# Kernel optimization log

Hardware: AMD Instinct MI355X
Metric: run time of the kernel (lower is better)

The kernel has to match this reference:

```python
import jax, jax.numpy as jnp
import numpy as np

NEG_BIG = -9e15

def setup_inputs() -> dict:
    key = jax.random.key(0)
    k1, k2, k3, k4 = jax.random.split(key, 4)
    N, F_in, F_out = 8192, 512, 128
    return {
        "input": jax.random.normal(k1, (N, F_in), dtype=jnp.float32),
        "adj": jax.random.randint(k2, (N, N), 0, 2, dtype=jnp.int32),
        "W": jax.random.normal(k3, (F_in, F_out), dtype=jnp.float32) * 0.05,
        "a": jax.random.normal(k4, (2 * F_out, 1), dtype=jnp.float32) * 0.05,
    }

def reference(input, adj, W, a):
    alpha = 0.2  # LeakyReLU negative slope
    h = input @ W                      # [N, F_out]
    F_out = h.shape[1]
    # concat score decomposition: a^T [h_i || h_j] = h_i @ a1 + h_j @ a2
    a1 = a[:F_out, 0]                  # [F_out]
    a2 = a[F_out:, 0]                  # [F_out]
    e = jax.nn.leaky_relu(h @ a1[:, None] + (h @ a2)[None, :], negative_slope=alpha)  # [N, N]
    e = jnp.where(adj > 0, e, NEG_BIG)
    attention = jax.nn.softmax(e, axis=1)
    h_prime = attention @ h            # [N, F_out]
    return jax.nn.elu(h_prime)         # concat=True
```

## Files before the change

### kernel.cpp

```cpp
#include <hip/hip_runtime.h>
#include <hip/hip_bf16.h>


typedef __attribute__((ext_vector_type(4))) float f32x4;
typedef __attribute__((ext_vector_type(8))) short s16x8;

#define N_NODES 8192
#define F_IN 512
#define F_OUT 128
#define JS 8
#define JCHUNK (N_NODES / JS)

static __device__ __forceinline__ short f2bf(float f) {
  __hip_bfloat16 h = __float2bfloat16(f);
  return __builtin_bit_cast(short, h);
}

__global__ __launch_bounds__(256) void k_mask(const int* __restrict__ adj,
    unsigned long long* __restrict__ mask) {
  const int nwaves = gridDim.x * 4;
  int wid = blockIdx.x * 4 + (threadIdx.x >> 6);
  int lane = threadIdx.x & 63;
  const int ntasks = N_NODES * (N_NODES / 64);
  for (int task = wid; task < ntasks; task += nwaves) {
    int row = task >> 7;
    int cg = task & 127;
    int v = adj[(size_t)row * N_NODES + cg * 64 + lane];
    unsigned long long b = __ballot(v != 0);
    if (lane == 0) mask[(size_t)row * (N_NODES / 64) + cg] = b;
  }
}

__global__ void k0a_wt(const float* __restrict__ W, unsigned short* __restrict__ WT) {
  int idx = blockIdx.x * 256 + threadIdx.x;
  int k = idx >> 7, f = idx & 127;
  WT[(size_t)f * F_IN + k] = (unsigned short)f2bf(W[idx]);
}

__global__ void k0c_wa(const float* __restrict__ W, const float* __restrict__ a,
                       float* __restrict__ wa) {
  int k = blockIdx.x * 256 + threadIdx.x;
  if (k >= F_IN) return;
  const float* Wr = W + (size_t)k * F_OUT;
  float d1 = 0.f, d2 = 0.f;
#pragma unroll 8
  for (int f = 0; f < F_OUT; f += 4) {
    f32x4 w  = *(const f32x4*)(Wr + f);
    f32x4 a1 = *(const f32x4*)(a + f);
    f32x4 a2 = *(const f32x4*)(a + F_OUT + f);
    d1 += w[0] * a1[0] + w[1] * a1[1] + w[2] * a1[2] + w[3] * a1[3];
    d2 += w[0] * a2[0] + w[1] * a2[1] + w[2] * a2[2] + w[3] * a2[3];
  }
  wa[k] = d1;
  wa[F_IN + k] = d2;
}

__global__ __launch_bounds__(256) void k0b_x(const float* __restrict__ X,
    const float* __restrict__ wa, unsigned short* __restrict__ Xb,
    f32x4* __restrict__ rowdat, unsigned* __restrict__ pE) {
  int wave = threadIdx.x >> 6, lane = threadIdx.x & 63;
  int i = blockIdx.x * 4 + wave;
  const float* Xr = X + (size_t)i * F_IN + lane * 8;
  f32x4 x0 = ((const f32x4*)Xr)[0];
  f32x4 x1 = ((const f32x4*)Xr)[1];
  f32x4 w10 = ((const f32x4*)(wa + lane * 8))[0];
  f32x4 w11 = ((const f32x4*)(wa + lane * 8))[1];
  f32x4 w20 = ((const f32x4*)(wa + F_IN + lane * 8))[0];
  f32x4 w21 = ((const f32x4*)(wa + F_IN + lane * 8))[1];

  s16x8 xb;
#pragma unroll
  for (int e = 0; e < 4; e++) { xb[e] = f2bf(x0[e]); xb[e + 4] = f2bf(x1[e]); }
  *(s16x8*)(Xb + (size_t)i * F_IN + lane * 8) = xb;

  float d1 = 0.f, d2 = 0.f;
#pragma unroll
  for (int e = 0; e < 4; e++) {
    d1 += x0[e] * w10[e] + x1[e] * w11[e];
    d2 += x0[e] * w20[e] + x1[e] * w21[e];
  }
#pragma unroll
  for (int m = 1; m < 64; m <<= 1) {
    d1 += __shfl_xor(d1, m, 64);
    d2 += __shfl_xor(d2, m, 64);
  }
  if (lane == 0) {
    float s1 = d1, s2 = d2;
    f32x4 rd;
    rd[0] = expf(s1);
    rd[1] = expf(0.2f * s1);
    rd[2] = expf(-s1);
    rd[3] = 0.f;
    rowdat[i] = rd;
    unsigned e2  = (unsigned)(unsigned short)f2bf(expf(s2));
    unsigned e2s = (unsigned)(unsigned short)f2bf(expf(0.2f * s2));
    pE[i] = (e2s << 16) | e2;
  }
}

__global__ __launch_bounds__(256) void k1_gemm(const unsigned short* __restrict__ WT,
    const unsigned short* __restrict__ Xb, unsigned short* __restrict__ hT) {
  int wave = threadIdx.x >> 6, lane = threadIdx.x & 63;
  int lrow = lane & 15, grp = lane >> 4;
  int tile = blockIdx.x * 4 + wave;
  int fb = tile & 7;
  int nb = tile >> 3;

  const unsigned short* Ar = WT + (size_t)(fb * 16 + lrow) * F_IN + grp * 8;
  const unsigned short* Br = Xb + (size_t)(nb * 16 + lrow) * F_IN + grp * 8;

  f32x4 acc = (f32x4)(0.0f);
#pragma unroll
  for (int k0 = 0; k0 < F_IN; k0 += 32) {
    s16x8 af = *(const s16x8*)(Ar + k0);
    s16x8 bf = *(const s16x8*)(Br + k0);
    acc = __builtin_amdgcn_mfma_f32_16x16x32_bf16(af, bf, acc, 0, 0, 0);
  }
#pragma unroll
  for (int r = 0; r < 4; r++)
    hT[(size_t)(fb * 16 + grp * 4 + r) * N_NODES + nb * 16 + lrow] =
        (unsigned short)f2bf(acc[r]);
}

__global__ __launch_bounds__(256, 4) void k2_main(const unsigned* __restrict__ mask32,
    const unsigned short* __restrict__ hT, const f32x4* __restrict__ rowdat,
    const unsigned* __restrict__ pE, float* __restrict__ accws,
    float* __restrict__ denws) {
  int js = blockIdx.x & (JS - 1);
  int rb = blockIdx.x / JS;
  int wave = threadIdx.x >> 6, lane = threadIdx.x & 63;
  int lrow = lane & 15, grp = lane >> 4;
  int waveRow = rb * 64 + wave * 16;
  int i0 = waveRow + lrow;
  int jlo = js * JCHUNK;

  f32x4 rd = rowdat[i0];
  float E1 = rd[0], E1s = rd[1], T1 = rd[2];

  f32x4 acc[8];
#pragma unroll
  for (int n = 0; n < 8; n++) acc[n] = (f32x4)(0.0f);
  float dsum = 0.f;

#define PROC(pe, e)                                                  \
  {                                                                  \
    unsigned pu = (pe);                                              \
    float E2  = __builtin_bit_cast(float, pu << 16);                 \
    float E2s = __builtin_bit_cast(float, pu & 0xffff0000u);         \
    float sel = (E2 > T1) ? E1 * E2 : E1s * E2s;                     \
    float p = ((b >> e) & 1u) ? sel : 0.f;                           \
    dsum += p;                                                       \
    af[e] = f2bf(p);                                                 \
  }

  for (int sc = 0; sc < JCHUNK / 512; sc++) {
    int jbase = jlo + sc * 512;
    const uint4* mrow =
        (const uint4*)(mask32 + (size_t)i0 * (N_NODES / 32) + jbase / 32);
    uint4 mm[4];
#pragma unroll
    for (int c = 0; c < 4; c++) mm[c] = mrow[c];

#pragma unroll
    for (int t = 0; t < 16; t++) {
      int jj = jbase + t * 32 + grp * 8;
      unsigned b = (mm[t >> 2][t & 3] >> (grp * 8)) & 0xffu;
      const uint4* pp = (const uint4*)(pE + jj);
      uint4 P0 = pp[0], P1 = pp[1];
      s16x8 af;
      PROC(P0.x, 0); PROC(P0.y, 1); PROC(P0.z, 2); PROC(P0.w, 3);
      PROC(P1.x, 4); PROC(P1.y, 5); PROC(P1.z, 6); PROC(P1.w, 7);
      const unsigned short* hTj = hT + jj;
#pragma unroll
      for (int n = 0; n < 8; n++) {
        s16x8 bf = *(const s16x8*)(hTj + (size_t)(n * 16 + lrow) * N_NODES);
        acc[n] = __builtin_amdgcn_mfma_f32_16x16x32_bf16(af, bf, acc[n], 0, 0, 0);
      }
    }
  }
#undef PROC

  dsum += __shfl_xor(dsum, 16, 64);
  dsum += __shfl_xor(dsum, 32, 64);
  if (lane < 16) denws[js * N_NODES + waveRow + lane] = dsum;

#pragma unroll
  for (int n = 0; n < 8; n++)
#pragma unroll
    for (int r = 0; r < 4; r++)
      accws[((size_t)js * N_NODES + waveRow + grp * 4 + r) * F_OUT + n * 16 + lrow] =
          acc[n][r];
}

__global__ void k3_fin(const float* __restrict__ accws,
                       const float* __restrict__ denws, float* __restrict__ out) {
  int idx4 = blockIdx.x * 256 + threadIdx.x;
  int i = idx4 >> 5;
  const int S4 = N_NODES * F_OUT / 4;
  f32x4 s = (f32x4)(0.0f);
  float d = 0.f;
#pragma unroll
  for (int js = 0; js < JS; js++) {
    s += ((const f32x4*)accws)[idx4 + js * S4];
    d += denws[i + js * N_NODES];
  }
  f32x4 v = s / d;
#pragma unroll
  for (int e = 0; e < 4; e++) v[e] = v[e] > 0.f ? v[e] : expm1f(v[e]);
  ((f32x4*)out)[idx4] = v;
}

extern "C" void kernel_launch(void* const* d_in, const int* in_sizes, int n_in,
                              void* d_out, int out_size, void* d_ws, size_t ws_size,
                              hipStream_t stream) {
  const float* X   = (const float*)d_in[0];
  const int*   adj = (const int*)d_in[1];
  const float* W   = (const float*)d_in[2];
  const float* a   = (const float*)d_in[3];
  float* out = (float*)d_out;

  char* ws = (char*)d_ws;
  size_t off = 0;
  unsigned short* WT = (unsigned short*)(ws + off); off += (size_t)F_OUT * F_IN * 2;
  unsigned short* Xb = (unsigned short*)(ws + off); off += (size_t)N_NODES * F_IN * 2;
  unsigned short* hT = (unsigned short*)(ws + off); off += (size_t)F_OUT * N_NODES * 2;
  f32x4* rowdat = (f32x4*)(ws + off); off += (size_t)N_NODES * 16;
  unsigned* pE = (unsigned*)(ws + off); off += (size_t)N_NODES * 4;
  float* wa = (float*)(ws + off); off += (size_t)2 * F_IN * 4;
  unsigned long long* mask = (unsigned long long*)(ws + off);
  off += (size_t)N_NODES * (N_NODES / 64) * 8;
  float* accws = (float*)(ws + off); off += (size_t)JS * N_NODES * F_OUT * 4;
  float* denws = (float*)(ws + off); off += (size_t)JS * N_NODES * 4;
  (void)in_sizes; (void)n_in; (void)out_size; (void)ws_size;

  k_mask<<<2048, 256, 0, stream>>>(adj, mask);
  k0a_wt<<<(F_IN * F_OUT) / 256, 256, 0, stream>>>(W, WT);
  k0c_wa<<<2, 256, 0, stream>>>(W, a, wa);
  k0b_x<<<N_NODES / 4, 256, 0, stream>>>(X, wa, Xb, rowdat, pE);
  k1_gemm<<<1024, 256, 0, stream>>>(WT, Xb, hT);
  k2_main<<<(N_NODES / 64) * JS, 256, 0, stream>>>((const unsigned*)mask, hT,
                                                   rowdat, pE, accws, denws);
  k3_fin<<<(N_NODES * F_OUT) / 4 / 256, 256, 0, stream>>>(accws, denws, out);
}
```

Measured before the change: 552.1 us.

## Give each wave 64 rows to reuse hT fragments across four MFMA row tiles

The main attention kernel now assigns each wave a 64-row by 512-column tile. Each hT B-fragment load feeds four MFMAs instead of one, which cuts global/L2 traffic for hT by about 4x. The j-split grows from 8 to 16, so the partial accumulator workspace and the final reduction double in size. Register use rises from 32 to 128 accumulator floats, and launch bounds drop occupancy to 2 blocks. Separately, the mask-building kernel has each wave handle 256 columns with four ballots and vectorized stores, reducing loop overhead.

```diff
diff --git a/kernel.cpp b/kernel.cpp
--- a/kernel.cpp
+++ b/kernel.cpp
@@ -8,8 +8,8 @@
 #define N_NODES 8192
 #define F_IN 512
 #define F_OUT 128
-#define JS 8
-#define JCHUNK (N_NODES / JS)
+#define JS 16
+#define WCOLS (N_NODES / JS)
 
 static __device__ __forceinline__ short f2bf(float f) {
   __hip_bfloat16 h = __float2bfloat16(f);
@@ -21,13 +21,23 @@
   const int nwaves = gridDim.x * 4;
   int wid = blockIdx.x * 4 + (threadIdx.x >> 6);
   int lane = threadIdx.x & 63;
-  const int ntasks = N_NODES * (N_NODES / 64);
+  const int ntasks = N_NODES * (N_NODES / 256);
   for (int task = wid; task < ntasks; task += nwaves) {
-    int row = task >> 7;
-    int cg = task & 127;
-    int v = adj[(size_t)row * N_NODES + cg * 64 + lane];
-    unsigned long long b = __ballot(v != 0);
-    if (lane == 0) mask[(size_t)row * (N_NODES / 64) + cg] = b;
+    int row = task >> 5;
+    int cg = task & 31;
+    const int* p = adj + (size_t)row * N_NODES + cg * 256 + lane;
+    int v0 = p[0], v1 = p[64], v2 = p[128], v3 = p[192];
+    unsigned long long b0 = __ballot(v0 != 0);
+    unsigned long long b1 = __ballot(v1 != 0);
+    unsigned long long b2 = __ballot(v2 != 0);
+    unsigned long long b3 = __ballot(v3 != 0);
+    if (lane == 0) {
+      unsigned long long* q = mask + (size_t)row * (N_NODES / 64) + cg * 4;
+      ulonglong2 w0; w0.x = b0; w0.y = b1;
+      ulonglong2 w1; w1.x = b2; w1.y = b3;
+      *(ulonglong2*)(q) = w0;
+      *(ulonglong2*)(q + 2) = w1;
+    }
   }
 }
 
@@ -122,74 +132,92 @@
         (unsigned short)f2bf(acc[r]);
 }
 
-__global__ __launch_bounds__(256, 4) void k2_main(const unsigned* __restrict__ mask32,
+__global__ __launch_bounds__(256, 2) void k2_main(const unsigned* __restrict__ mask32,
     const unsigned short* __restrict__ hT, const f32x4* __restrict__ rowdat,
     const unsigned* __restrict__ pE, float* __restrict__ accws,
     float* __restrict__ denws) {
-  int js = blockIdx.x & (JS - 1);
-  int rb = blockIdx.x / JS;
   int wave = threadIdx.x >> 6, lane = threadIdx.x & 63;
   int lrow = lane & 15, grp = lane >> 4;
-  int waveRow = rb * 64 + wave * 16;
-  int i0 = waveRow + lrow;
-  int jlo = js * JCHUNK;
-
-  f32x4 rd = rowdat[i0];
-  float E1 = rd[0], E1s = rd[1], T1 = rd[2];
-
-  f32x4 acc[8];
-#pragma unroll
-  for (int n = 0; n < 8; n++) acc[n] = (f32x4)(0.0f);
-  float dsum = 0.f;
-
-#define PROC(pe, e)                                                  \
-  {                                                                  \
-    unsigned pu = (pe);                                              \
-    float E2  = __builtin_bit_cast(float, pu << 16);                 \
-    float E2s = __builtin_bit_cast(float, pu & 0xffff0000u);         \
-    float sel = (E2 > T1) ? E1 * E2 : E1s * E2s;                     \
-    float p = ((b >> e) & 1u) ? sel : 0.f;                           \
-    dsum += p;                                                       \
-    af[e] = f2bf(p);                                                 \
-  }
-
-  for (int sc = 0; sc < JCHUNK / 512; sc++) {
-    int jbase = jlo + sc * 512;
-    const uint4* mrow =
-        (const uint4*)(mask32 + (size_t)i0 * (N_NODES / 32) + jbase / 32);
+  int rb = blockIdx.x >> 2;
+  int js = (blockIdx.x & 3) * 4 + wave;
+  int rbase = rb * 64;
+  int jlo = js * WCOLS;
+
+  float E1[4], E1s[4], T1[4];
+#pragma unroll
+  for (int rt = 0; rt < 4; rt++) {
+    f32x4 rd = rowdat[rbase + rt * 16 + lrow];
+    E1[rt] = rd[0]; E1s[rt] = rd[1]; T1[rt] = rd[2];
+  }
+
+  f32x4 acc[4][8];
+#pragma unroll
+  for (int rt = 0; rt < 4; rt++)
+#pragma unroll
+    for (int n = 0; n < 8; n++) acc[rt][n] = (f32x4)(0.0f);
+  float dsum[4] = {0.f, 0.f, 0.f, 0.f};
+
+#define PROC1(rt, pe, e)                                              \
+  {                                                                   \
+    unsigned pu = (pe);                                               \
+    float E2  = __builtin_bit_cast(float, pu << 16);                  \
+    float E2s = __builtin_bit_cast(float, pu & 0xffff0000u);          \
+    float sel = (E2 > T1[rt]) ? E1[rt] * E2 : E1s[rt] * E2s;          \
+    float p = ((b >> (e)) & 1u) ? sel : 0.f;                          \
+    dsum[rt] += p;                                                    \
+    af[rt][e] = f2bf(p);                                              \
+  }
+
+  for (int sc = 0; sc < 4; sc++) {
+    int jb = jlo + sc * 128;
     uint4 mm[4];
 #pragma unroll
-    for (int c = 0; c < 4; c++) mm[c] = mrow[c];
-
-#pragma unroll
-    for (int t = 0; t < 16; t++) {
-      int jj = jbase + t * 32 + grp * 8;
-      unsigned b = (mm[t >> 2][t & 3] >> (grp * 8)) & 0xffu;
+    for (int rt = 0; rt < 4; rt++)
+      mm[rt] = *(const uint4*)(mask32 +
+          (size_t)(rbase + rt * 16 + lrow) * (N_NODES / 32) + jb / 32);
+
+#pragma unroll
+    for (int t = 0; t < 4; t++) {
+      int jj = jb + t * 32 + grp * 8;
       const uint4* pp = (const uint4*)(pE + jj);
       uint4 P0 = pp[0], P1 = pp[1];
-      s16x8 af;
-      PROC(P0.x, 0); PROC(P0.y, 1); PROC(P0.z, 2); PROC(P0.w, 3);
-      PROC(P1.x, 4); PROC(P1.y, 5); PROC(P1.z, 6); PROC(P1.w, 7);
-      const unsigned short* hTj = hT + jj;
+      s16x8 af[4];
+#pragma unroll
+      for (int rt = 0; rt < 4; rt++) {
+        unsigned b = (mm[rt][t] >> (grp * 8)) & 0xffu;
+        PROC1(rt, P0.x, 0); PROC1(rt, P0.y, 1);
+        PROC1(rt, P0.z, 2); PROC1(rt, P0.w, 3);
+        PROC1(rt, P1.x, 4); PROC1(rt, P1.y, 5);
+        PROC1(rt, P1.z, 6); PROC1(rt, P1.w, 7);
+      }
 #pragma unroll
       for (int n = 0; n < 8; n++) {
-        s16x8 bf = *(const s16x8*)(hTj + (size_t)(n * 16 + lrow) * N_NODES);
-        acc[n] = __builtin_amdgcn_mfma_f32_16x16x32_bf16(af, bf, acc[n], 0, 0, 0);
+        s16x8 bf = *(const s16x8*)(hT + (size_t)(n * 16 + lrow) * N_NODES + jj);
+#pragma unroll
+        for (int rt = 0; rt < 4; rt++)
+          acc[rt][n] =
+              __builtin_amdgcn_mfma_f32_16x16x32_bf16(af[rt], bf, acc[rt][n], 0, 0, 0);
       }
     }
   }
-#undef PROC
-
-  dsum += __shfl_xor(dsum, 16, 64);
-  dsum += __shfl_xor(dsum, 32, 64);
-  if (lane < 16) denws[js * N_NODES + waveRow + lane] = dsum;
-
-#pragma unroll
-  for (int n = 0; n < 8; n++)
-#pragma unroll
-    for (int r = 0; r < 4; r++)
-      accws[((size_t)js * N_NODES + waveRow + grp * 4 + r) * F_OUT + n * 16 + lrow] =
-          acc[n][r];
+#undef PROC1
+
+#pragma unroll
+  for (int rt = 0; rt < 4; rt++) {
+    float d = dsum[rt];
+    d += __shfl_xor(d, 16, 64);
+    d += __shfl_xor(d, 32, 64);
+    if (lane < 16) denws[js * N_NODES + rbase + rt * 16 + lane] = d;
+  }
+
+#pragma unroll
+  for (int rt = 0; rt < 4; rt++)
+#pragma unroll
+    for (int n = 0; n < 8; n++)
+#pragma unroll
+      for (int r = 0; r < 4; r++)
+        accws[((size_t)js * N_NODES + rbase + rt * 16 + grp * 4 + r) * F_OUT +
+              n * 16 + lrow] = acc[rt][n][r];
 }
 
 __global__ void k3_fin(const float* __restrict__ accws,
@@ -201,7 +229,7 @@
   float d = 0.f;
 #pragma unroll
   for (int js = 0; js < JS; js++) {
-    s += ((const f32x4*)accws)[idx4 + js * S4];
+    s += ((const f32x4*)accws)[idx4 + (size_t)js * S4];
     d += denws[i + js * N_NODES];
   }
   f32x4 v = s / d;
@@ -238,7 +266,7 @@
   k0c_wa<<<2, 256, 0, stream>>>(W, a, wa);
   k0b_x<<<N_NODES / 4, 256, 0, stream>>>(X, wa, Xb, rowdat, pE);
   k1_gemm<<<1024, 256, 0, stream>>>(WT, Xb, hT);
-  k2_main<<<(N_NODES / 64) * JS, 256, 0, stream>>>((const unsigned*)mask, hT,
-                                                   rowdat, pE, accws, denws);
+  k2_main<<<(N_NODES / 64) * (JS / 4), 256, 0, stream>>>((const unsigned*)mask, hT,
+                                                         rowdat, pE, accws, denws);
   k3_fin<<<(N_NODES * F_OUT) / 4 / 256, 256, 0, stream>>>(accws, denws, out);
 }
```

Result: faster. 535.8 us (-2.9%).
